# Optimization experiments

Hardware: AMD Instinct MI355X
Metric: run time of the kernel (lower is better)

## Reference

```python
import jax, jax.numpy as jnp
import numpy as np

X_SCALE = 20.0
THR = 0.25
BETA = 15.0
DT = 1.0
GAIN = 1.0


def setup_inputs() -> dict:
    key = jax.random.key(0)
    k1, k2, k3 = jax.random.split(key, 3)
    x = jax.random.normal(k1, (32, 1, 8192), dtype=jnp.float32)
    conv_w = jax.random.normal(k2, (64, 1, 8), dtype=jnp.float32)
    raw_tau = jax.random.normal(k3, (64,), dtype=jnp.float32)
    return {"x": x, "conv_w": conv_w, "raw_tau": raw_tau}


def _forward(x, conv_w, raw_tau):
    K = conv_w.shape[-1]
    # normalize each filter to unit norm (clamp_min 1e-8)
    norms = jnp.linalg.norm(conv_w.reshape(conv_w.shape[0], -1), axis=1)
    w = conv_w / jnp.maximum(norms, 1e-8)[:, None, None]
    # causal conv: left-pad by K-1
    I = GAIN * jax.lax.conv_general_dilated(
        X_SCALE * x, w, window_strides=(1,), padding=[(K - 1, 0)],
        dimension_numbers=("NCH", "OIH", "NCH"))  # (B, F, L)
    tau = jax.nn.softplus(raw_tau) + 1e-4
    alpha = jnp.exp(-DT / tau).astype(I.dtype)  # (F,)

    def step(v, I_t):
        v_pre = alpha * v + (1.0 - alpha) * I_t  # (B, F)
        z = BETA * (v_pre - THR)
        s = (v_pre >= THR).astype(I_t.dtype)  # hard spike, no grad
        v_new = v_pre * (1.0 - s)  # reset where spiked
        return v_new, (z, s)

    I_tfirst = jnp.transpose(I, (2, 0, 1))  # (L, B, F)
    v0 = jnp.zeros(I.shape[:2], dtype=I.dtype)  # (B, F)
    _, (z, s) = jax.lax.scan(step, v0, I_tfirst)
    z = jnp.transpose(z, (1, 2, 0))  # (B, F, L)
    s = jnp.transpose(s, (1, 2, 0))
    logits = jnp.max(z, axis=1)  # (B, L)
    return I, z, s, logits


def reference(x, conv_w, raw_tau):
    return _forward(x, conv_w, raw_tau)
```

## Files before the change

### kernel.cpp

```cpp
#include <hip/hip_runtime.h>
#include <math.h>


#define LL 8192
#define BB 32
#define FF 64
#define KK 8
#define CHUNK 128
#define NCH 64
#define WARM 96
#define NX (WARM + 7 + CHUNK)
#define TS 32
#define NT (CHUNK / TS)

typedef float f32x4 __attribute__((ext_vector_type(4)));

__global__ __launch_bounds__(64) void snn_kernel(
    const float* __restrict__ x, const float* __restrict__ conv_w,
    const float* __restrict__ raw_tau, float* __restrict__ out)
{
    __shared__ float x_lds[NX + 1];
    __shared__ float I_tile[FF][TS + 1];
    __shared__ float z_tile[FF][TS + 1];

    const int f  = threadIdx.x;
    const int b  = blockIdx.y;
    const int c  = blockIdx.x;
    const int t0 = c * CHUNK;
    const int g0 = t0 - WARM - 7;

    double wdd[KK];
    double ss = 0.0;
    #pragma unroll
    for (int k = 0; k < KK; ++k) {
        double wv = (double)conv_w[f * KK + k];
        wdd[k] = wv;
        ss += wv * wv;
    }
    double nrm = sqrt(ss);
    if (nrm < 1e-8) nrm = 1e-8;
    double invn = 1.0 / nrm;
    float wf[KK];
    #pragma unroll
    for (int k = 0; k < KK; ++k) wf[k] = (float)(wdd[k] * invn);

    double rt     = (double)raw_tau[f];
    double tau    = log1p(exp(rt)) + 1e-4;
    double alphad = exp(-1.0 / tau);
    float alpha = (float)alphad;
    float oma   = (float)(1.0 - alphad);

    for (int i = f; i < NX; i += 64) {
        int g = g0 + i;
        x_lds[i] = (g >= 0) ? (20.0f * x[(size_t)b * LL + g]) : 0.0f;
    }

    float* outI  = out;
    float* outZ  = out + (size_t)BB * FF * LL;
    float* outS  = out + (size_t)2 * BB * FF * LL;
    float* outLg = out + (size_t)3 * BB * FF * LL;

    float v = 0.0f;

    #pragma unroll 8
    for (int s = 0; s < WARM; ++s) {
        float acc = 0.0f;
        #pragma unroll
        for (int k = 0; k < KK; ++k) acc = fmaf(wf[k], x_lds[s + k], acc);
        float vp = fmaf(alpha, v, oma * acc);
        v = (vp >= 0.25f) ? 0.0f : vp;
    }

    for (int tile = 0; tile < NT; ++tile) {
        #pragma unroll
        for (int j = 0; j < TS; ++j) {
            int s = WARM + tile * TS + j;
            float acc = 0.0f;
            #pragma unroll
            for (int k = 0; k < KK; ++k) acc = fmaf(wf[k], x_lds[s + k], acc);
            float vp = fmaf(alpha, v, oma * acc);
            float z  = fmaf(15.0f, vp, -3.75f);
            I_tile[f][j] = acc;
            z_tile[f][j] = z;
            v = (vp >= 0.25f) ? 0.0f : vp;
        }

        const int gt = t0 + tile * TS;
        {
            int r = f >> 3;
            int q = (f & 7) * 4;
            #pragma unroll
            for (int it = 0; it < 8; ++it) {
                int fr = it * 8 + r;
                size_t base = ((size_t)b * FF + fr) * LL + gt + q;
                f32x4 vi = { I_tile[fr][q], I_tile[fr][q + 1],
                             I_tile[fr][q + 2], I_tile[fr][q + 3] };
                f32x4 vz = { z_tile[fr][q], z_tile[fr][q + 1],
                             z_tile[fr][q + 2], z_tile[fr][q + 3] };
                f32x4 vs = { vz.x >= 0.f ? 1.f : 0.f,
                             vz.y >= 0.f ? 1.f : 0.f,
                             vz.z >= 0.f ? 1.f : 0.f,
                             vz.w >= 0.f ? 1.f : 0.f };
                __builtin_nontemporal_store(vi, reinterpret_cast<f32x4*>(outI + base));
                __builtin_nontemporal_store(vz, reinterpret_cast<f32x4*>(outZ + base));
                __builtin_nontemporal_store(vs, reinterpret_cast<f32x4*>(outS + base));
            }
            int t = f & 31, g = f >> 5;
            float m = z_tile[g * 32][t];
            #pragma unroll
            for (int i = 1; i < 32; ++i) m = fmaxf(m, z_tile[g * 32 + i][t]);
            m = fmaxf(m, __shfl_xor(m, 32));
            if (f < 32) outLg[(size_t)b * LL + gt + f] = m;
        }
    }
}

extern "C" void kernel_launch(void* const* d_in, const int* in_sizes, int n_in,
                              void* d_out, int out_size, void* d_ws, size_t ws_size,
                              hipStream_t stream) {
    const float* x  = (const float*)d_in[0];
    const float* w  = (const float*)d_in[1];
    const float* rt = (const float*)d_in[2];
    float* out = (float*)d_out;
    dim3 grid(NCH, BB);
    snn_kernel<<<grid, 64, 0, stream>>>(x, w, rt, out);
}
```

Baseline: 215.6 us.

## Double-buffer tile staging and rebuild I from stored membrane potential

The scan now writes only the pre-reset potential vp to LDS, using alternating double buffers. I is recovered during the flush as (vp_t - alpha*v_{t-1})/(1-alpha), and z, s and the logits are derived from vp. This halves the per-step LDS writes in the serial recurrence and lets the compute of one tile overlap the store phase of the previous one. Reconstructing I algebraically can differ from the directly computed conv output by rounding, especially when alpha is close to 1.

After: 217.4 us. Within noise of the previous version (+0.8%).

```diff
diff --git a/kernel.cpp b/kernel.cpp
--- a/kernel.cpp
+++ b/kernel.cpp
@@ -12,6 +12,7 @@
 #define NX (WARM + 7 + CHUNK)
 #define TS 32
 #define NT (CHUNK / TS)
+#define TSP (TS + 3)
 
 typedef float f32x4 __attribute__((ext_vector_type(4)));
 
@@ -20,8 +21,10 @@
     const float* __restrict__ raw_tau, float* __restrict__ out)
 {
     __shared__ float x_lds[NX + 1];
-    __shared__ float I_tile[FF][TS + 1];
-    __shared__ float z_tile[FF][TS + 1];
+    __shared__ float vpA[FF][TSP];
+    __shared__ float vpB[FF][TSP];
+    __shared__ float alpha_s[FF];
+    __shared__ float ioma_s[FF];
 
     const int f  = threadIdx.x;
     const int b  = blockIdx.y;
@@ -30,14 +33,14 @@
     const int g0 = t0 - WARM - 7;
 
     double wdd[KK];
-    double ss = 0.0;
+    double ssum = 0.0;
     #pragma unroll
     for (int k = 0; k < KK; ++k) {
         double wv = (double)conv_w[f * KK + k];
         wdd[k] = wv;
-        ss += wv * wv;
+        ssum += wv * wv;
     }
-    double nrm = sqrt(ss);
+    double nrm = sqrt(ssum);
     if (nrm < 1e-8) nrm = 1e-8;
     double invn = 1.0 / nrm;
     float wf[KK];
@@ -47,8 +50,10 @@
     double rt     = (double)raw_tau[f];
     double tau    = log1p(exp(rt)) + 1e-4;
     double alphad = exp(-1.0 / tau);
-    float alpha = (float)alphad;
-    float oma   = (float)(1.0 - alphad);
+    const float alpha = (float)alphad;
+    const float oma   = (float)(1.0 - alphad);
+    alpha_s[f] = alpha;
+    ioma_s[f]  = (float)(1.0 / (1.0 - alphad));
 
     for (int i = f; i < NX; i += 64) {
         int g = g0 + i;
@@ -60,7 +65,7 @@
     float* outS  = out + (size_t)2 * BB * FF * LL;
     float* outLg = out + (size_t)3 * BB * FF * LL;
 
-    float v = 0.0f;
+    float v = 0.0f, vp_last = 0.0f;
 
     #pragma unroll 8
     for (int s = 0; s < WARM; ++s) {
@@ -68,10 +73,12 @@
         #pragma unroll
         for (int k = 0; k < KK; ++k) acc = fmaf(wf[k], x_lds[s + k], acc);
         float vp = fmaf(alpha, v, oma * acc);
+        vp_last = vp;
         v = (vp >= 0.25f) ? 0.0f : vp;
     }
 
-    for (int tile = 0; tile < NT; ++tile) {
+    auto compute_tile = [&](int tile, float (*buf)[TSP]) {
+        buf[f][0] = vp_last;
         #pragma unroll
         for (int j = 0; j < TS; ++j) {
             int s = WARM + tile * TS + j;
@@ -79,40 +86,68 @@
             #pragma unroll
             for (int k = 0; k < KK; ++k) acc = fmaf(wf[k], x_lds[s + k], acc);
             float vp = fmaf(alpha, v, oma * acc);
-            float z  = fmaf(15.0f, vp, -3.75f);
-            I_tile[f][j] = acc;
-            z_tile[f][j] = z;
+            buf[f][j + 1] = vp;
+            vp_last = vp;
             v = (vp >= 0.25f) ? 0.0f : vp;
         }
+    };
 
+    auto flush_tile = [&](int tile, float (*buf)[TSP]) {
         const int gt = t0 + tile * TS;
-        {
-            int r = f >> 3;
-            int q = (f & 7) * 4;
-            #pragma unroll
-            for (int it = 0; it < 8; ++it) {
-                int fr = it * 8 + r;
-                size_t base = ((size_t)b * FF + fr) * LL + gt + q;
-                f32x4 vi = { I_tile[fr][q], I_tile[fr][q + 1],
-                             I_tile[fr][q + 2], I_tile[fr][q + 3] };
-                f32x4 vz = { z_tile[fr][q], z_tile[fr][q + 1],
-                             z_tile[fr][q + 2], z_tile[fr][q + 3] };
-                f32x4 vs = { vz.x >= 0.f ? 1.f : 0.f,
-                             vz.y >= 0.f ? 1.f : 0.f,
-                             vz.z >= 0.f ? 1.f : 0.f,
-                             vz.w >= 0.f ? 1.f : 0.f };
-                __builtin_nontemporal_store(vi, reinterpret_cast<f32x4*>(outI + base));
-                __builtin_nontemporal_store(vz, reinterpret_cast<f32x4*>(outZ + base));
-                __builtin_nontemporal_store(vs, reinterpret_cast<f32x4*>(outS + base));
+        const int r = f >> 3;
+        const int q = (f & 7) * 4;
+        #pragma unroll
+        for (int it = 0; it < 8; ++it) {
+            int fr = it * 8 + r;
+            float al = alpha_s[fr];
+            float io = ioma_s[fr];
+            size_t base = ((size_t)b * FF + fr) * LL + gt + q;
+            float p0 = buf[fr][q + 0];
+            float p1 = buf[fr][q + 1];
+            float p2 = buf[fr][q + 2];
+            float p3 = buf[fr][q + 3];
+            float p4 = buf[fr][q + 4];
+            f32x4 vi, vz, vs;
+            {
+                float vprev = (p0 >= 0.25f) ? 0.0f : p0;
+                vi.x = fmaf(-al, vprev, p1) * io;
+                vz.x = fmaf(15.0f, p1, -3.75f);
+                vs.x = (p1 >= 0.25f) ? 1.0f : 0.0f;
             }
-            int t = f & 31, g = f >> 5;
-            float m = z_tile[g * 32][t];
-            #pragma unroll
-            for (int i = 1; i < 32; ++i) m = fmaxf(m, z_tile[g * 32 + i][t]);
-            m = fmaxf(m, __shfl_xor(m, 32));
-            if (f < 32) outLg[(size_t)b * LL + gt + f] = m;
+            {   float vprev = (p1 >= 0.25f) ? 0.0f : p1;
+                vi.y = fmaf(-al, vprev, p2) * io;
+                vz.y = fmaf(15.0f, p2, -3.75f);
+                vs.y = (p2 >= 0.25f) ? 1.0f : 0.0f;
+            }
+            {   float vprev = (p2 >= 0.25f) ? 0.0f : p2;
+                vi.z = fmaf(-al, vprev, p3) * io;
+                vz.z = fmaf(15.0f, p3, -3.75f);
+                vs.z = (p3 >= 0.25f) ? 1.0f : 0.0f;
+            }
+            {   float vprev = (p3 >= 0.25f) ? 0.0f : p3;
+                vi.w = fmaf(-al, vprev, p4) * io;
+                vz.w = fmaf(15.0f, p4, -3.75f);
+                vs.w = (p4 >= 0.25f) ? 1.0f : 0.0f;
+            }
+            __builtin_nontemporal_store(vi, reinterpret_cast<f32x4*>(outI + base));
+            __builtin_nontemporal_store(vz, reinterpret_cast<f32x4*>(outZ + base));
+            __builtin_nontemporal_store(vs, reinterpret_cast<f32x4*>(outS + base));
         }
+        int t = f & 31, g = f >> 5;
+        float m = buf[g * 32][t + 1];
+        #pragma unroll
+        for (int i = 1; i < 32; ++i) m = fmaxf(m, buf[g * 32 + i][t + 1]);
+        m = fmaxf(m, __shfl_xor(m, 32));
+        if (f < 32) outLg[(size_t)b * LL + gt + f] = fmaf(15.0f, m, -3.75f);
+    };
+
+    compute_tile(0, vpA);
+    #pragma unroll
+    for (int tile = 1; tile < NT; ++tile) {
+        if (tile & 1) { compute_tile(tile, vpB); flush_tile(tile - 1, vpA); }
+        else          { compute_tile(tile, vpA); flush_tile(tile - 1, vpB); }
     }
+    flush_tile(NT - 1, ((NT - 1) & 1) ? vpB : vpA);
 }
 
 extern "C" void kernel_launch(void* const* d_in, const int* in_sizes, int n_in,
```

## Store only membrane potential per step and reconstruct outputs in a separate write phase

Applied to the files above, without the earlier changes.

Doubles the chunk length per block and halves the grid. Blocks are remapped through a swizzled chunk index. During the recurrence the loop now stores only the pre-reset potential to shared memory, instead of both I and z in 32-step tiles. A separate write phase then recovers I algebraically as (vp - alpha*vprev)/(1-alpha), derives z and s from vp, computes the logits max from vp, and writes all outputs with vectorized nontemporal stores. The aim is to decouple the serial scan from the global stores and cut LDS traffic, at the cost of fewer blocks and possible float rounding differences in the reconstructed I when 1-alpha is small.

After: 234.9 us. 1.09x slower.

```diff
diff --git a/kernel.cpp b/kernel.cpp
--- a/kernel.cpp
+++ b/kernel.cpp
@@ -6,12 +6,11 @@
 #define BB 32
 #define FF 64
 #define KK 8
-#define CHUNK 128
-#define NCH 64
+#define CHUNK 256
+#define NCH 32
 #define WARM 96
 #define NX (WARM + 7 + CHUNK)
-#define TS 32
-#define NT (CHUNK / TS)
+#define VPW (CHUNK + 1)
 
 typedef float f32x4 __attribute__((ext_vector_type(4)));
 
@@ -19,25 +18,27 @@
     const float* __restrict__ x, const float* __restrict__ conv_w,
     const float* __restrict__ raw_tau, float* __restrict__ out)
 {
+    __shared__ float vp_s[FF][VPW];
     __shared__ float x_lds[NX + 1];
-    __shared__ float I_tile[FF][TS + 1];
-    __shared__ float z_tile[FF][TS + 1];
+    __shared__ float alpha_s[FF];
+    __shared__ float ioma_s[FF];
 
     const int f  = threadIdx.x;
     const int b  = blockIdx.y;
-    const int c  = blockIdx.x;
+    const int i  = blockIdx.x;
+    const int c  = (i & 7) * (NCH / 8) + (i >> 3);
     const int t0 = c * CHUNK;
     const int g0 = t0 - WARM - 7;
 
     double wdd[KK];
-    double ss = 0.0;
+    double ssum = 0.0;
     #pragma unroll
     for (int k = 0; k < KK; ++k) {
         double wv = (double)conv_w[f * KK + k];
         wdd[k] = wv;
-        ss += wv * wv;
+        ssum += wv * wv;
     }
-    double nrm = sqrt(ss);
+    double nrm = sqrt(ssum);
     if (nrm < 1e-8) nrm = 1e-8;
     double invn = 1.0 / nrm;
     float wf[KK];
@@ -47,12 +48,14 @@
     double rt     = (double)raw_tau[f];
     double tau    = log1p(exp(rt)) + 1e-4;
     double alphad = exp(-1.0 / tau);
-    float alpha = (float)alphad;
-    float oma   = (float)(1.0 - alphad);
+    const float alpha = (float)alphad;
+    const float oma   = (float)(1.0 - alphad);
+    alpha_s[f] = alpha;
+    ioma_s[f]  = (float)(1.0 / (1.0 - alphad));
 
-    for (int i = f; i < NX; i += 64) {
-        int g = g0 + i;
-        x_lds[i] = (g >= 0) ? (20.0f * x[(size_t)b * LL + g]) : 0.0f;
+    for (int idx = f; idx < NX; idx += 64) {
+        int g = g0 + idx;
+        x_lds[idx] = (g >= 0) ? (20.0f * x[(size_t)b * LL + g]) : 0.0f;
     }
 
     float* outI  = out;
@@ -68,51 +71,60 @@
         #pragma unroll
         for (int k = 0; k < KK; ++k) acc = fmaf(wf[k], x_lds[s + k], acc);
         float vp = fmaf(alpha, v, oma * acc);
+        if (s == WARM - 1) vp_s[f][0] = vp;
         v = (vp >= 0.25f) ? 0.0f : vp;
     }
 
-    for (int tile = 0; tile < NT; ++tile) {
+    #pragma unroll 8
+    for (int t = 0; t < CHUNK; ++t) {
+        int s = WARM + t;
+        float acc = 0.0f;
         #pragma unroll
-        for (int j = 0; j < TS; ++j) {
-            int s = WARM + tile * TS + j;
-            float acc = 0.0f;
-            #pragma unroll
-            for (int k = 0; k < KK; ++k) acc = fmaf(wf[k], x_lds[s + k], acc);
-            float vp = fmaf(alpha, v, oma * acc);
-            float z  = fmaf(15.0f, vp, -3.75f);
-            I_tile[f][j] = acc;
-            z_tile[f][j] = z;
-            v = (vp >= 0.25f) ? 0.0f : vp;
-        }
+        for (int k = 0; k < KK; ++k) acc = fmaf(wf[k], x_lds[s + k], acc);
+        float vp = fmaf(alpha, v, oma * acc);
+        vp_s[f][1 + t] = vp;
+        v = (vp >= 0.25f) ? 0.0f : vp;
+    }
 
-        const int gt = t0 + tile * TS;
-        {
-            int r = f >> 3;
-            int q = (f & 7) * 4;
-            #pragma unroll
-            for (int it = 0; it < 8; ++it) {
-                int fr = it * 8 + r;
-                size_t base = ((size_t)b * FF + fr) * LL + gt + q;
-                f32x4 vi = { I_tile[fr][q], I_tile[fr][q + 1],
-                             I_tile[fr][q + 2], I_tile[fr][q + 3] };
-                f32x4 vz = { z_tile[fr][q], z_tile[fr][q + 1],
-                             z_tile[fr][q + 2], z_tile[fr][q + 3] };
-                f32x4 vs = { vz.x >= 0.f ? 1.f : 0.f,
-                             vz.y >= 0.f ? 1.f : 0.f,
-                             vz.z >= 0.f ? 1.f : 0.f,
-                             vz.w >= 0.f ? 1.f : 0.f };
-                __builtin_nontemporal_store(vi, reinterpret_cast<f32x4*>(outI + base));
-                __builtin_nontemporal_store(vz, reinterpret_cast<f32x4*>(outZ + base));
-                __builtin_nontemporal_store(vs, reinterpret_cast<f32x4*>(outS + base));
-            }
-            int t = f & 31, g = f >> 5;
-            float m = z_tile[g * 32][t];
-            #pragma unroll
-            for (int i = 1; i < 32; ++i) m = fmaxf(m, z_tile[g * 32 + i][t]);
-            m = fmaxf(m, __shfl_xor(m, 32));
-            if (f < 32) outLg[(size_t)b * LL + gt + f] = m;
-        }
+    const int tq = 4 * f;
+    f32x4 mx = { -1e30f, -1e30f, -1e30f, -1e30f };
+    #pragma unroll 4
+    for (int fr = 0; fr < FF; ++fr) {
+        float al = alpha_s[fr];
+        float io = ioma_s[fr];
+        f32x4 p  = *reinterpret_cast<f32x4*>(&vp_s[fr][1 + tq]);
+        float pm1 = vp_s[fr][tq];
+        f32x4 vi, vz, vs;
+        {   float vprev = (pm1 >= 0.25f) ? 0.0f : pm1;
+            vi.x = fmaf(-al, vprev, p.x) * io;
+            vz.x = fmaf(15.0f, p.x, -3.75f);
+            vs.x = (p.x >= 0.25f) ? 1.0f : 0.0f; }
+        {   float vprev = (p.x >= 0.25f) ? 0.0f : p.x;
+            vi.y = fmaf(-al, vprev, p.y) * io;
+            vz.y = fmaf(15.0f, p.y, -3.75f);
+            vs.y = (p.y >= 0.25f) ? 1.0f : 0.0f; }
+        {   float vprev = (p.y >= 0.25f) ? 0.0f : p.y;
+            vi.z = fmaf(-al, vprev, p.z) * io;
+            vz.z = fmaf(15.0f, p.z, -3.75f);
+            vs.z = (p.z >= 0.25f) ? 1.0f : 0.0f; }
+        {   float vprev = (p.z >= 0.25f) ? 0.0f : p.z;
+            vi.w = fmaf(-al, vprev, p.w) * io;
+            vz.w = fmaf(15.0f, p.w, -3.75f);
+            vs.w = (p.w >= 0.25f) ? 1.0f : 0.0f; }
+        mx.x = fmaxf(mx.x, p.x); mx.y = fmaxf(mx.y, p.y);
+        mx.z = fmaxf(mx.z, p.z); mx.w = fmaxf(mx.w, p.w);
+        size_t base = ((size_t)b * FF + fr) * LL + t0 + tq;
+        __builtin_nontemporal_store(vi, reinterpret_cast<f32x4*>(outI + base));
+        __builtin_nontemporal_store(vz, reinterpret_cast<f32x4*>(outZ + base));
+        __builtin_nontemporal_store(vs, reinterpret_cast<f32x4*>(outS + base));
     }
+    f32x4 lg;
+    lg.x = fmaf(15.0f, mx.x, -3.75f);
+    lg.y = fmaf(15.0f, mx.y, -3.75f);
+    lg.z = fmaf(15.0f, mx.z, -3.75f);
+    lg.w = fmaf(15.0f, mx.w, -3.75f);
+    __builtin_nontemporal_store(lg,
+        reinterpret_cast<f32x4*>(outLg + (size_t)b * LL + t0 + tq));
 }
 
 extern "C" void kernel_launch(void* const* d_in, const int* in_sizes, int n_in,
```

## Pipeline scan with previous tile's output flush, rebuild I from stored v_pre

Applied to the files above, without the earlier changes.

Interleaves the recurrence scan of each 32-step tile with the global stores of the previous tile, using double-buffered LDS tiles. Only v_pre goes to LDS; I, z and s are rebuilt from it (I by inverting the update with 1/(1-alpha)). The conv input window is kept in registers and filled from vectorised LDS loads, and the warm-up length drops from 96 to 64 steps. Stores become scalar 4-byte nontemporal writes instead of float4. The shorter warm-up and the reconstruction of I can change results relative to the reference, especially for filters with alpha near 1.

Measured after the change: 215.5 us. Within noise of the previous version (-0.1%).

```diff
diff --git a/kernel.cpp b/kernel.cpp
--- a/kernel.cpp
+++ b/kernel.cpp
@@ -8,10 +8,11 @@
 #define KK 8
 #define CHUNK 128
 #define NCH 64
-#define WARM 96
+#define WARM 64
 #define NX (WARM + 7 + CHUNK)
 #define TS 32
 #define NT (CHUNK / TS)
+#define ROWW (TS + 1)
 
 typedef float f32x4 __attribute__((ext_vector_type(4)));
 
@@ -19,25 +20,29 @@
     const float* __restrict__ x, const float* __restrict__ conv_w,
     const float* __restrict__ raw_tau, float* __restrict__ out)
 {
-    __shared__ float x_lds[NX + 1];
-    __shared__ float I_tile[FF][TS + 1];
-    __shared__ float z_tile[FF][TS + 1];
+    __shared__ __align__(16) float x_lds[NX + 9];
+    __shared__ float bufA[FF][ROWW];
+    __shared__ float bufB[FF][ROWW];
+    __shared__ float alpha_s[FF];
+    __shared__ float ioma_s[FF];
 
-    const int f  = threadIdx.x;
-    const int b  = blockIdx.y;
-    const int c  = blockIdx.x;
-    const int t0 = c * CHUNK;
-    const int g0 = t0 - WARM - 7;
+    const int f    = threadIdx.x;
+    const int b    = blockIdx.y;
+    const int c    = blockIdx.x;
+    const int t0   = c * CHUNK;
+    const int g0   = t0 - WARM - 7;
+    const int tl   = f & 31;
+    const int half = f >> 5;
 
     double wdd[KK];
-    double ss = 0.0;
+    double ssum = 0.0;
     #pragma unroll
     for (int k = 0; k < KK; ++k) {
         double wv = (double)conv_w[f * KK + k];
         wdd[k] = wv;
-        ss += wv * wv;
+        ssum += wv * wv;
     }
-    double nrm = sqrt(ss);
+    double nrm = sqrt(ssum);
     if (nrm < 1e-8) nrm = 1e-8;
     double invn = 1.0 / nrm;
     float wf[KK];
@@ -47,12 +52,14 @@
     double rt     = (double)raw_tau[f];
     double tau    = log1p(exp(rt)) + 1e-4;
     double alphad = exp(-1.0 / tau);
-    float alpha = (float)alphad;
-    float oma   = (float)(1.0 - alphad);
+    const float alpha_f = (float)alphad;
+    const float oma     = (float)(1.0 - alphad);
+    alpha_s[f] = alpha_f;
+    ioma_s[f]  = (float)(1.0 / (1.0 - alphad));
 
-    for (int i = f; i < NX; i += 64) {
+    for (int i = f; i < NX + 8; i += 64) {
         int g = g0 + i;
-        x_lds[i] = (g >= 0) ? (20.0f * x[(size_t)b * LL + g]) : 0.0f;
+        x_lds[i] = (i < NX && g >= 0) ? (20.0f * x[(size_t)b * LL + g]) : 0.0f;
     }
 
     float* outI  = out;
@@ -60,58 +67,113 @@
     float* outS  = out + (size_t)2 * BB * FF * LL;
     float* outLg = out + (size_t)3 * BB * FF * LL;
 
-    float v = 0.0f;
+    float v = 0.0f, vp_last = 0.0f;
+    float xw[16];
+    {
+        f32x4 a  = *(const f32x4*)&x_lds[0];
+        f32x4 b4 = *(const f32x4*)&x_lds[4];
+        xw[0]=a.x; xw[1]=a.y; xw[2]=a.z; xw[3]=a.w;
+        xw[4]=b4.x; xw[5]=b4.y; xw[6]=b4.z; xw[7]=b4.w;
+    }
+    #define LOAD8(base) do { \
+        f32x4 _a  = *(const f32x4*)&x_lds[(base)];     \
+        f32x4 _b4 = *(const f32x4*)&x_lds[(base) + 4]; \
+        xw[8]=_a.x; xw[9]=_a.y; xw[10]=_a.z; xw[11]=_a.w; \
+        xw[12]=_b4.x; xw[13]=_b4.y; xw[14]=_b4.z; xw[15]=_b4.w; } while (0)
+    #define SHIFT8() do { _Pragma("unroll") \
+        for (int _i = 0; _i < 8; ++_i) xw[_i] = xw[_i + 8]; } while (0)
+    #define SCAN_STEP(J) \
+        float acc = 0.0f; \
+        _Pragma("unroll") \
+        for (int _k = 0; _k < KK; ++_k) acc = fmaf(wf[_k], xw[(J) + _k], acc); \
+        float vp = fmaf(alpha_f, v, oma * acc); \
+        vp_last = vp; \
+        v = (vp >= 0.25f) ? 0.0f : vp;
 
-    #pragma unroll 8
-    for (int s = 0; s < WARM; ++s) {
-        float acc = 0.0f;
+    #pragma unroll
+    for (int m = 0; m < WARM / 8; ++m) {
+        LOAD8(8 * m + 8);
         #pragma unroll
-        for (int k = 0; k < KK; ++k) acc = fmaf(wf[k], x_lds[s + k], acc);
-        float vp = fmaf(alpha, v, oma * acc);
-        v = (vp >= 0.25f) ? 0.0f : vp;
+        for (int j = 0; j < 8; ++j) { SCAN_STEP(j); }
+        SHIFT8();
     }
 
-    for (int tile = 0; tile < NT; ++tile) {
+    bufA[f][0] = vp_last;
+    #pragma unroll
+    for (int m = 0; m < 4; ++m) {
+        LOAD8(WARM + 8 * m + 8);
         #pragma unroll
-        for (int j = 0; j < TS; ++j) {
-            int s = WARM + tile * TS + j;
-            float acc = 0.0f;
+        for (int j = 0; j < 8; ++j) {
+            SCAN_STEP(j);
+            bufA[f][1 + 8 * m + j] = vp;
+        }
+        SHIFT8();
+    }
+
+    float mx;
+    auto tile_scan_flush = [&](int k, float (*cur)[ROWW], float (*prev)[ROWW]) {
+        cur[f][0] = vp_last;
+        const int gtp = t0 + (k - 1) * TS;
+        mx = -1e30f;
+        #pragma unroll
+        for (int m = 0; m < 4; ++m) {
+            LOAD8(WARM + k * TS + 8 * m + 8);
             #pragma unroll
-            for (int k = 0; k < KK; ++k) acc = fmaf(wf[k], x_lds[s + k], acc);
-            float vp = fmaf(alpha, v, oma * acc);
-            float z  = fmaf(15.0f, vp, -3.75f);
-            I_tile[f][j] = acc;
-            z_tile[f][j] = z;
-            v = (vp >= 0.25f) ? 0.0f : vp;
+            for (int j = 0; j < 8; ++j) {
+                {   SCAN_STEP(j);
+                    cur[f][1 + 8 * m + j] = vp;
+                }
+                int   q   = 8 * m + j;
+                int   row = 2 * q + half;
+                float pb  = prev[row][1 + tl];
+                float pm  = prev[row][tl];
+                float al  = alpha_s[row];
+                float io2 = ioma_s[row];
+                float vprev = (pm >= 0.25f) ? 0.0f : pm;
+                float Iv = fmaf(-al, vprev, pb) * io2;
+                float zv = fmaf(15.0f, pb, -3.75f);
+                float sv = (pb >= 0.25f) ? 1.0f : 0.0f;
+                size_t basep = ((size_t)b * FF + row) * LL + gtp + tl;
+                __builtin_nontemporal_store(Iv, outI + basep);
+                __builtin_nontemporal_store(zv, outZ + basep);
+                __builtin_nontemporal_store(sv, outS + basep);
+                mx = fmaxf(mx, pb);
+            }
+            SHIFT8();
         }
+        float m2 = fmaxf(mx, __shfl_xor(mx, 32));
+        if (half == 0)
+            __builtin_nontemporal_store(fmaf(15.0f, m2, -3.75f),
+                                        outLg + (size_t)b * LL + gtp + tl);
+    };
+    tile_scan_flush(1, bufB, bufA);
+    tile_scan_flush(2, bufA, bufB);
+    tile_scan_flush(3, bufB, bufA);
 
-        const int gt = t0 + tile * TS;
-        {
-            int r = f >> 3;
-            int q = (f & 7) * 4;
-            #pragma unroll
-            for (int it = 0; it < 8; ++it) {
-                int fr = it * 8 + r;
-                size_t base = ((size_t)b * FF + fr) * LL + gt + q;
-                f32x4 vi = { I_tile[fr][q], I_tile[fr][q + 1],
-                             I_tile[fr][q + 2], I_tile[fr][q + 3] };
-                f32x4 vz = { z_tile[fr][q], z_tile[fr][q + 1],
-                             z_tile[fr][q + 2], z_tile[fr][q + 3] };
-                f32x4 vs = { vz.x >= 0.f ? 1.f : 0.f,
-                             vz.y >= 0.f ? 1.f : 0.f,
-                             vz.z >= 0.f ? 1.f : 0.f,
-                             vz.w >= 0.f ? 1.f : 0.f };
-                __builtin_nontemporal_store(vi, reinterpret_cast<f32x4*>(outI + base));
-                __builtin_nontemporal_store(vz, reinterpret_cast<f32x4*>(outZ + base));
-                __builtin_nontemporal_store(vs, reinterpret_cast<f32x4*>(outS + base));
-            }
-            int t = f & 31, g = f >> 5;
-            float m = z_tile[g * 32][t];
-            #pragma unroll
-            for (int i = 1; i < 32; ++i) m = fmaxf(m, z_tile[g * 32 + i][t]);
-            m = fmaxf(m, __shfl_xor(m, 32));
-            if (f < 32) outLg[(size_t)b * LL + gt + f] = m;
+    {
+        const int gtp = t0 + 3 * TS;
+        mx = -1e30f;
+        #pragma unroll
+        for (int q = 0; q < 32; ++q) {
+            int   row = 2 * q + half;
+            float pb  = bufB[row][1 + tl];
+            float pm  = bufB[row][tl];
+            float al  = alpha_s[row];
+            float io2 = ioma_s[row];
+            float vprev = (pm >= 0.25f) ? 0.0f : pm;
+            float Iv = fmaf(-al, vprev, pb) * io2;
+            float zv = fmaf(15.0f, pb, -3.75f);
+            float sv = (pb >= 0.25f) ? 1.0f : 0.0f;
+            size_t basep = ((size_t)b * FF + row) * LL + gtp + tl;
+            __builtin_nontemporal_store(Iv, outI + basep);
+            __builtin_nontemporal_store(zv, outZ + basep);
+            __builtin_nontemporal_store(sv, outS + basep);
+            mx = fmaxf(mx, pb);
         }
+        float m2 = fmaxf(mx, __shfl_xor(mx, 32));
+        if (half == 0)
+            __builtin_nontemporal_store(fmaf(15.0f, m2, -3.75f),
+                                        outLg + (size_t)b * LL + gtp + tl);
     }
 }
 
```
